# Kernel tuning notes

Hardware: AMD Instinct MI355X
Metric: run time of the kernel (lower is better)

## Reference

```python
import jax, jax.numpy as jnp
import numpy as np

DIM = 192
WH, WW = 8, 8
N = WH * WW
NUM_HEADS = 6
HEAD_DIM = DIM // NUM_HEADS
SCALE = HEAD_DIM ** (-0.5)
B_ = 4096


def _relative_position_index(Wh, Ww):
    coords = np.stack(np.meshgrid(np.arange(Wh), np.arange(Ww), indexing='ij'))  # [2, Wh, Ww]
    cf = coords.reshape(2, -1)                              # [2, N]
    rel = cf[:, :, None] - cf[:, None, :]                   # [2, N, N]
    rel = rel.transpose(1, 2, 0).astype(np.int64)           # [N, N, 2]
    rel[..., 0] += Wh - 1
    rel[..., 1] += Ww - 1
    rel[..., 0] *= 2 * Ww - 1
    return rel.sum(-1)                                      # [N, N]


REL_IDX = jnp.asarray(_relative_position_index(WH, WW))


def setup_inputs() -> dict:
    key = jax.random.key(0)
    ks = jax.random.split(key, 6)
    x = jax.random.normal(ks[0], (B_, N, DIM), dtype=jnp.float32)
    w_qkv = jax.random.normal(ks[1], (3 * DIM, DIM), dtype=jnp.float32) * (DIM ** -0.5)
    b_qkv = jnp.zeros((3 * DIM,), dtype=jnp.float32)
    w_proj = jax.random.normal(ks[2], (DIM, DIM), dtype=jnp.float32) * (DIM ** -0.5)
    b_proj = jnp.zeros((DIM,), dtype=jnp.float32)
    # torch init is zeros; use small noise so the bias path is exercised
    bias_table = jax.random.normal(ks[3], ((2 * WH - 1) * (2 * WW - 1), NUM_HEADS), dtype=jnp.float32) * 0.02
    return {"x": x, "w_qkv": w_qkv, "b_qkv": b_qkv, "w_proj": w_proj,
            "b_proj": b_proj, "bias_table": bias_table}


def reference(x, w_qkv, b_qkv, w_proj, b_proj, bias_table):
    B, n, C = x.shape
    qkv = jnp.einsum('bnc,dc->bnd', x, w_qkv) + b_qkv        # [B, N, 3C]
    qkv = qkv.reshape(B, n, 3, NUM_HEADS, HEAD_DIM)
    q = qkv[:, :, 0].transpose(0, 2, 1, 3) * SCALE            # [B, H, N, hd]
    k = qkv[:, :, 1].transpose(0, 2, 1, 3)
    v = qkv[:, :, 2].transpose(0, 2, 1, 3)
    attn = jnp.einsum('bhnd,bhmd->bhnm', q, k)                # [B, H, N, N]
    bias = bias_table[REL_IDX]                                # [N, N, H]
    attn = attn + bias.transpose(2, 0, 1)[None]               # broadcast over B
    attn = jax.nn.softmax(attn, axis=-1)
    out = jnp.einsum('bhnm,bhmd->bnhd', attn, v).reshape(B, n, C)
    return jnp.einsum('bnc,dc->bnd', out, w_proj) + b_proj
```

## Files before the change

kernel.cpp:

```cpp
#include <hip/hip_runtime.h>

#define TOK 64
#define CDIM 192
#define NH 6
#define HD 32
#define THREADS 768
#define QSCALE 0.17677669529663687f

#define WQ16_OFF 0
#define WP16_OFF 110592
#define BIAS_OFF 147456
#define WS_HALFS (147456 + 24576)
#define WS_BYTES (WS_HALFS * 2)

typedef _Float16 f16x8 __attribute__((ext_vector_type(8)));
typedef _Float16 f16x4 __attribute__((ext_vector_type(4)));
typedef float f32x4 __attribute__((ext_vector_type(4)));

__device__ __forceinline__ f16x8 ld8(const _Float16* p) {
  return *reinterpret_cast<const f16x8*>(p);
}

__device__ __forceinline__ f16x8 cvt8(const float* __restrict__ p) {
  float4 a = *reinterpret_cast<const float4*>(p);
  float4 c = *reinterpret_cast<const float4*>(p + 4);
  f16x8 r;
  r[0] = (_Float16)a.x; r[1] = (_Float16)a.y; r[2] = (_Float16)a.z; r[3] = (_Float16)a.w;
  r[4] = (_Float16)c.x; r[5] = (_Float16)c.y; r[6] = (_Float16)c.z; r[7] = (_Float16)c.w;
  return r;
}

__global__ void prep_ws(const float* __restrict__ wq, const float* __restrict__ wp,
                        const float* __restrict__ bt, _Float16* __restrict__ ws) {
  int i = blockIdx.x * 256 + threadIdx.x;
  if (i < 27648) {
    float4 v = reinterpret_cast<const float4*>(wq)[i];
    f16x4 h;
    h[0] = (_Float16)v.x; h[1] = (_Float16)v.y; h[2] = (_Float16)v.z; h[3] = (_Float16)v.w;
    *reinterpret_cast<f16x4*>(ws + WQ16_OFF + (size_t)i * 4) = h;
  } else if (i < 36864) {
    int j = i - 27648;
    float4 v = reinterpret_cast<const float4*>(wp)[j];
    f16x4 h;
    h[0] = (_Float16)v.x; h[1] = (_Float16)v.y; h[2] = (_Float16)v.z; h[3] = (_Float16)v.w;
    *reinterpret_cast<f16x4*>(ws + WP16_OFF + (size_t)j * 4) = h;
  } else if (i < 61440) {
    int j = i - 36864;
    int hit = j >> 10;
    int l = (j >> 4) & 63;
    int s = j & 15;
    int h = hit >> 2, it = hit & 3;
    int ii = it * 16 + (l & 15);
    int jj = (s >> 2) * 16 + (l >> 4) * 4 + (s & 3);
    int rel = ((ii >> 3) - (jj >> 3) + 7) * 15 + ((ii & 7) - (jj & 7) + 7);
    ws[BIAS_OFF + j] = (_Float16)bt[rel * NH + h];
  }
}

template <bool WS>
__global__ __launch_bounds__(THREADS, 6) void winattn(
    const float* __restrict__ x, const float* __restrict__ w_qkv,
    const float* __restrict__ b_qkv, const float* __restrict__ w_proj,
    const float* __restrict__ b_proj, const float* __restrict__ bias_table,
    const _Float16* __restrict__ ws, float* __restrict__ out) {
  __shared__ __align__(16) _Float16 R1[12288];
  __shared__ __align__(16) _Float16 R2[12288];

  const int tid = threadIdx.x;
  const int w   = tid >> 6;
  const int l   = tid & 63;
  const int l15 = l & 15;
  const int lg  = l >> 4;
  const int b   = blockIdx.x;
  const int h   = w >> 1;
  const int wh  = w & 1;
  const f32x4 vzero = {0.f, 0.f, 0.f, 0.f};

  const float* xg = x + (size_t)b * (TOK * CDIM);
#pragma unroll
  for (int i = tid; i < TOK * CDIM / 4; i += THREADS) {
    int n = i / (CDIM / 4);
    int c = (i % (CDIM / 4)) * 4;
    float4 v = reinterpret_cast<const float4*>(xg)[i];
    f16x4 h4;
    h4[0] = (_Float16)v.x; h4[1] = (_Float16)v.y;
    h4[2] = (_Float16)v.z; h4[3] = (_Float16)v.w;
    *reinterpret_cast<f16x4*>(&R1[((c >> 3) * TOK + n) * 8 + (c & 7)]) = h4;
  }
  __syncthreads();

  const int sdl = h * HD + wh * 16 + l15;
  const int hd  = wh * 16 + l15;

  f32x4 aq[4], ak[4];
#pragma unroll
  for (int mt = 0; mt < 4; ++mt) { aq[mt] = vzero; ak[mt] = vzero; }
#pragma unroll
  for (int ks = 0; ks < 6; ++ks) {
    f16x8 a[4];
#pragma unroll
    for (int mt = 0; mt < 4; ++mt)
      a[mt] = ld8(&R1[((ks * 4 + lg) * TOK + mt * 16 + l15) * 8]);
    f16x8 bfq, bfk;
    if constexpr (WS) {
      bfq = ld8(ws + WQ16_OFF + (size_t)sdl * CDIM + ks * 32 + lg * 8);
      bfk = ld8(ws + WQ16_OFF + (size_t)(CDIM + sdl) * CDIM + ks * 32 + lg * 8);
    } else {
      bfq = cvt8(w_qkv + (size_t)sdl * CDIM + ks * 32 + lg * 8);
      bfk = cvt8(w_qkv + (size_t)(CDIM + sdl) * CDIM + ks * 32 + lg * 8);
    }
#pragma unroll
    for (int mt = 0; mt < 4; ++mt) {
      aq[mt] = __builtin_amdgcn_mfma_f32_16x16x32_f16(a[mt], bfq, aq[mt], 0, 0, 0);
      ak[mt] = __builtin_amdgcn_mfma_f32_16x16x32_f16(a[mt], bfk, ak[mt], 0, 0, 0);
    }
  }
  {
    float bq1 = b_qkv[CDIM + sdl];
#pragma unroll
    for (int mt = 0; mt < 4; ++mt)
#pragma unroll
      for (int r = 0; r < 4; ++r) {
        int n = mt * 16 + lg * 4 + r;
        R2[h * 2048 + ((hd >> 3) * TOK + n) * 8 + (hd & 7)] = (_Float16)(ak[mt][r] + bq1);
      }
  }

  f32x4 av[4];
#pragma unroll
  for (int mt = 0; mt < 4; ++mt) av[mt] = vzero;
#pragma unroll
  for (int ks = 0; ks < 6; ++ks) {
    f16x8 a[4];
#pragma unroll
    for (int mt = 0; mt < 4; ++mt)
      a[mt] = ld8(&R1[((ks * 4 + lg) * TOK + mt * 16 + l15) * 8]);
    f16x8 bfv;
    if constexpr (WS) bfv = ld8(ws + WQ16_OFF + (size_t)(2 * CDIM + sdl) * CDIM + ks * 32 + lg * 8);
    else              bfv = cvt8(w_qkv + (size_t)(2 * CDIM + sdl) * CDIM + ks * 32 + lg * 8);
#pragma unroll
    for (int mt = 0; mt < 4; ++mt)
      av[mt] = __builtin_amdgcn_mfma_f32_16x16x32_f16(a[mt], bfv, av[mt], 0, 0, 0);
  }
  __syncthreads();

  f16x8 kf[4];
#pragma unroll
  for (int jt = 0; jt < 4; ++jt)
    kf[jt] = ld8(&R2[h * 2048 + (lg * TOK + jt * 16 + l15) * 8]);
  {
    float bq2 = b_qkv[2 * CDIM + sdl];
#pragma unroll
    for (int mt = 0; mt < 4; ++mt)
#pragma unroll
      for (int r = 0; r < 4; ++r) {
        int n = mt * 16 + lg * 4 + r;
        R1[h * 2048 + ((n >> 3) * HD + hd) * 8 + (n & 7)] = (_Float16)(av[mt][r] + bq2);
      }
  }
  __syncthreads();

  f16x8 vf[4];
#pragma unroll
  for (int z = 0; z < 4; ++z) {
    int ks = z >> 1, nt = z & 1;
    vf[z] = ld8(&R1[h * 2048 + ((ks * 4 + lg) * HD + nt * 16 + l15) * 8]);
  }
  {
    float bq0 = b_qkv[sdl];
#pragma unroll
    for (int mt = 0; mt < 4; ++mt)
#pragma unroll
      for (int r = 0; r < 4; ++r) {
        int n = mt * 16 + lg * 4 + r;
        R2[h * 2048 + ((hd >> 3) * TOK + n) * 8 + (hd & 7)] =
            (_Float16)((aq[mt][r] + bq0) * QSCALE);
      }
  }
  __syncthreads();

  f16x8 qf[2];
#pragma unroll
  for (int ii = 0; ii < 2; ++ii) {
    int it = wh * 2 + ii;
    qf[ii] = ld8(&R2[h * 2048 + (lg * TOK + it * 16 + l15) * 8]);
  }
  __syncthreads();

  {
    _Float16* pbase = &R2[w * 1024];
#pragma unroll
    for (int ii = 0; ii < 2; ++ii) {
      const int it = wh * 2 + ii;
      f32x4 st[4];
#pragma unroll
      for (int jt = 0; jt < 4; ++jt)
        st[jt] = __builtin_amdgcn_mfma_f32_16x16x32_f16(kf[jt], qf[ii], vzero, 0, 0, 0);
      if constexpr (WS) {
        const _Float16* bw = ws + BIAS_OFF + ((h * 4 + it) * 64 + l) * 16;
        f16x8 b0 = ld8(bw), b1 = ld8(bw + 8);
#pragma unroll
        for (int jt = 0; jt < 4; ++jt)
#pragma unroll
          for (int r = 0; r < 4; ++r)
            st[jt][r] += (float)((jt < 2) ? b0[jt * 4 + r] : b1[(jt - 2) * 4 + r]);
      } else {
        int i = it * 16 + l15, yi = i >> 3, xi = i & 7;
#pragma unroll
        for (int jt = 0; jt < 4; ++jt)
#pragma unroll
          for (int r = 0; r < 4; ++r) {
            int j = jt * 16 + lg * 4 + r, yj = j >> 3, xj = j & 7;
            st[jt][r] += bias_table[(((yi - yj + 7) * 15 + (xi - xj + 7)) * NH + h)];
          }
      }
      float m = st[0][0];
#pragma unroll
      for (int jt = 0; jt < 4; ++jt)
#pragma unroll
        for (int r = 0; r < 4; ++r) m = fmaxf(m, st[jt][r]);
      m = fmaxf(m, __shfl_xor(m, 16, 64));
      m = fmaxf(m, __shfl_xor(m, 32, 64));
      float sum = 0.f;
#pragma unroll
      for (int jt = 0; jt < 4; ++jt)
#pragma unroll
        for (int r = 0; r < 4; ++r) { st[jt][r] = __expf(st[jt][r] - m); sum += st[jt][r]; }
      sum += __shfl_xor(sum, 16, 64);
      sum += __shfl_xor(sum, 32, 64);
      float inv = 1.f / sum;
#pragma unroll
      for (int jt = 0; jt < 4; ++jt) {
        f16x4 pk;
#pragma unroll
        for (int r = 0; r < 4; ++r) pk[r] = (_Float16)(st[jt][r] * inv);
        *reinterpret_cast<f16x4*>(
            &pbase[((jt * 2 + (lg >> 1)) * 16 + l15) * 8 + (lg & 1) * 4]) = pk;
      }
      f32x4 o[2] = {vzero, vzero};
#pragma unroll
      for (int ks = 0; ks < 2; ++ks) {
        f16x8 pf = ld8(&pbase[((ks * 4 + lg) * 16 + l15) * 8]);
#pragma unroll
        for (int nt = 0; nt < 2; ++nt)
          o[nt] = __builtin_amdgcn_mfma_f32_16x16x32_f16(pf, vf[ks * 2 + nt], o[nt], 0, 0, 0);
      }
#pragma unroll
      for (int nt = 0; nt < 2; ++nt) {
        int c = h * HD + nt * 16 + l15;
#pragma unroll
        for (int r = 0; r < 4; ++r) {
          int i2 = it * 16 + lg * 4 + r;
          R1[((c >> 3) * TOK + i2) * 8 + (c & 7)] = (_Float16)o[nt][r];
        }
      }
    }
  }
  __syncthreads();

  {
    const int e = w * 16 + l15;
    f32x4 pacc[4];
#pragma unroll
    for (int mt = 0; mt < 4; ++mt) pacc[mt] = vzero;
#pragma unroll
    for (int ks = 0; ks < 6; ++ks) {
      f16x8 bf;
      if constexpr (WS) bf = ld8(ws + WP16_OFF + (size_t)e * CDIM + ks * 32 + lg * 8);
      else              bf = cvt8(w_proj + (size_t)e * CDIM + ks * 32 + lg * 8);
#pragma unroll
      for (int mt = 0; mt < 4; ++mt) {
        f16x8 a = ld8(&R1[((ks * 4 + lg) * TOK + mt * 16 + l15) * 8]);
        pacc[mt] = __builtin_amdgcn_mfma_f32_16x16x32_f16(a, bf, pacc[mt], 0, 0, 0);
      }
    }
    float bp = b_proj[e];
#pragma unroll
    for (int mt = 0; mt < 4; ++mt)
#pragma unroll
      for (int r = 0; r < 4; ++r) {
        int n = mt * 16 + lg * 4 + r;
        out[((size_t)b * TOK + n) * CDIM + e] = pacc[mt][r] + bp;
      }
  }
}

extern "C" void kernel_launch(void* const* d_in, const int* in_sizes, int n_in,
                              void* d_out, int out_size, void* d_ws, size_t ws_size,
                              hipStream_t stream) {
  const float* x          = (const float*)d_in[0];
  const float* w_qkv      = (const float*)d_in[1];
  const float* b_qkv      = (const float*)d_in[2];
  const float* w_proj     = (const float*)d_in[3];
  const float* b_proj     = (const float*)d_in[4];
  const float* bias_table = (const float*)d_in[5];
  float* out = (float*)d_out;
  int B = in_sizes[0] / (TOK * CDIM);

  if (ws_size >= (size_t)WS_BYTES) {
    _Float16* ws = (_Float16*)d_ws;
    hipLaunchKernelGGL(prep_ws, dim3(240), dim3(256), 0, stream,
                       w_qkv, w_proj, bias_table, ws);
    hipLaunchKernelGGL(winattn<true>, dim3(B), dim3(THREADS), 0, stream,
                       x, w_qkv, b_qkv, w_proj, b_proj, bias_table, ws, out);
  } else {
    hipLaunchKernelGGL(winattn<false>, dim3(B), dim3(THREADS), 0, stream,
                       x, w_qkv, b_qkv, w_proj, b_proj, bias_table,
                       (const _Float16*)nullptr, out);
  }
}
```

Baseline: 213.6 us.

## Swizzle LDS tile layouts to cut bank conflicts, add MFMA priority hints

Applies an XOR swizzle on the row index to every shared-memory tile (x, K, Q, V, attention output) and changes the matching reads and writes. The x staging loop now writes 8 halves per store, and the V store is vectorised to 4-half writes, so LDS bank conflicts and store count both drop. It also wraps the MFMA groups in s_setprio to favour matrix issue across waves. This adds index arithmetic, and any mismatch in the swizzle between writers and readers would corrupt results.

```diff
diff --git a/kernel.cpp b/kernel.cpp
--- a/kernel.cpp
+++ b/kernel.cpp
@@ -78,29 +78,36 @@
 
   const float* xg = x + (size_t)b * (TOK * CDIM);
 #pragma unroll
-  for (int i = tid; i < TOK * CDIM / 4; i += THREADS) {
-    int n = i / (CDIM / 4);
-    int c = (i % (CDIM / 4)) * 4;
-    float4 v = reinterpret_cast<const float4*>(xg)[i];
-    f16x4 h4;
-    h4[0] = (_Float16)v.x; h4[1] = (_Float16)v.y;
-    h4[2] = (_Float16)v.z; h4[3] = (_Float16)v.w;
-    *reinterpret_cast<f16x4*>(&R1[((c >> 3) * TOK + n) * 8 + (c & 7)]) = h4;
+  for (int kk = 0; kk < 2; ++kk) {
+    int q = tid + kk * 768;
+    int n = q / 24;
+    int p = q - n * 24;
+    const float* src = xg + q * 8;
+    float4 v0 = *reinterpret_cast<const float4*>(src);
+    float4 v1 = *reinterpret_cast<const float4*>(src + 4);
+    f16x8 h8;
+    h8[0] = (_Float16)v0.x; h8[1] = (_Float16)v0.y;
+    h8[2] = (_Float16)v0.z; h8[3] = (_Float16)v0.w;
+    h8[4] = (_Float16)v1.x; h8[5] = (_Float16)v1.y;
+    h8[6] = (_Float16)v1.z; h8[7] = (_Float16)v1.w;
+    *reinterpret_cast<f16x8*>(&R1[(p * TOK + (n ^ (p & 7))) * 8]) = h8;
   }
   __syncthreads();
 
   const int sdl = h * HD + wh * 16 + l15;
   const int hd  = wh * 16 + l15;
+  const int dp  = hd >> 3;
 
   f32x4 aq[4], ak[4];
 #pragma unroll
   for (int mt = 0; mt < 4; ++mt) { aq[mt] = vzero; ak[mt] = vzero; }
 #pragma unroll
   for (int ks = 0; ks < 6; ++ks) {
+    const int sp = (ks * 4) & 7;
     f16x8 a[4];
 #pragma unroll
     for (int mt = 0; mt < 4; ++mt)
-      a[mt] = ld8(&R1[((ks * 4 + lg) * TOK + mt * 16 + l15) * 8]);
+      a[mt] = ld8(&R1[((ks * 4 + lg) * TOK + ((mt * 16 + l15) ^ (sp + lg))) * 8]);
     f16x8 bfq, bfk;
     if constexpr (WS) {
       bfq = ld8(ws + WQ16_OFF + (size_t)sdl * CDIM + ks * 32 + lg * 8);
@@ -109,11 +116,13 @@
       bfq = cvt8(w_qkv + (size_t)sdl * CDIM + ks * 32 + lg * 8);
       bfk = cvt8(w_qkv + (size_t)(CDIM + sdl) * CDIM + ks * 32 + lg * 8);
     }
+    __builtin_amdgcn_s_setprio(1);
 #pragma unroll
     for (int mt = 0; mt < 4; ++mt) {
       aq[mt] = __builtin_amdgcn_mfma_f32_16x16x32_f16(a[mt], bfq, aq[mt], 0, 0, 0);
       ak[mt] = __builtin_amdgcn_mfma_f32_16x16x32_f16(a[mt], bfk, ak[mt], 0, 0, 0);
     }
+    __builtin_amdgcn_s_setprio(0);
   }
   {
     float bq1 = b_qkv[CDIM + sdl];
@@ -122,7 +131,7 @@
 #pragma unroll
       for (int r = 0; r < 4; ++r) {
         int n = mt * 16 + lg * 4 + r;
-        R2[h * 2048 + ((hd >> 3) * TOK + n) * 8 + (hd & 7)] = (_Float16)(ak[mt][r] + bq1);
+        R2[h * 2048 + (dp * TOK + (n ^ dp)) * 8 + (hd & 7)] = (_Float16)(ak[mt][r] + bq1);
       }
   }
 
@@ -131,49 +140,55 @@
   for (int mt = 0; mt < 4; ++mt) av[mt] = vzero;
 #pragma unroll
   for (int ks = 0; ks < 6; ++ks) {
+    const int sp = (ks * 4) & 7;
     f16x8 a[4];
 #pragma unroll
     for (int mt = 0; mt < 4; ++mt)
-      a[mt] = ld8(&R1[((ks * 4 + lg) * TOK + mt * 16 + l15) * 8]);
+      a[mt] = ld8(&R1[((ks * 4 + lg) * TOK + ((mt * 16 + l15) ^ (sp + lg))) * 8]);
     f16x8 bfv;
     if constexpr (WS) bfv = ld8(ws + WQ16_OFF + (size_t)(2 * CDIM + sdl) * CDIM + ks * 32 + lg * 8);
     else              bfv = cvt8(w_qkv + (size_t)(2 * CDIM + sdl) * CDIM + ks * 32 + lg * 8);
+    __builtin_amdgcn_s_setprio(1);
 #pragma unroll
     for (int mt = 0; mt < 4; ++mt)
       av[mt] = __builtin_amdgcn_mfma_f32_16x16x32_f16(a[mt], bfv, av[mt], 0, 0, 0);
+    __builtin_amdgcn_s_setprio(0);
   }
   __syncthreads();
 
   f16x8 kf[4];
 #pragma unroll
   for (int jt = 0; jt < 4; ++jt)
-    kf[jt] = ld8(&R2[h * 2048 + (lg * TOK + jt * 16 + l15) * 8]);
+    kf[jt] = ld8(&R2[h * 2048 + (lg * TOK + ((jt * 16 + l15) ^ lg)) * 8]);
   {
     float bq2 = b_qkv[2 * CDIM + sdl];
+#pragma unroll
+    for (int mt = 0; mt < 4; ++mt) {
+      int vp = 2 * mt + (lg >> 1);
+      f16x4 pk;
+#pragma unroll
+      for (int r = 0; r < 4; ++r) pk[r] = (_Float16)(av[mt][r] + bq2);
+      *reinterpret_cast<f16x4*>(
+          &R1[h * 2048 + (vp * HD + (hd ^ vp)) * 8 + (lg & 1) * 4]) = pk;
+    }
+  }
+  __syncthreads();
+
+  f16x8 vf[4];
+#pragma unroll
+  for (int z = 0; z < 4; ++z) {
+    int ks = z >> 1, nt = z & 1;
+    int tp = ks * 4 + lg;
+    vf[z] = ld8(&R1[h * 2048 + (tp * HD + ((nt * 16 + l15) ^ tp)) * 8]);
+  }
+  {
+    float bq0 = b_qkv[sdl];
 #pragma unroll
     for (int mt = 0; mt < 4; ++mt)
 #pragma unroll
       for (int r = 0; r < 4; ++r) {
         int n = mt * 16 + lg * 4 + r;
-        R1[h * 2048 + ((n >> 3) * HD + hd) * 8 + (n & 7)] = (_Float16)(av[mt][r] + bq2);
-      }
-  }
-  __syncthreads();
-
-  f16x8 vf[4];
-#pragma unroll
-  for (int z = 0; z < 4; ++z) {
-    int ks = z >> 1, nt = z & 1;
-    vf[z] = ld8(&R1[h * 2048 + ((ks * 4 + lg) * HD + nt * 16 + l15) * 8]);
-  }
-  {
-    float bq0 = b_qkv[sdl];
-#pragma unroll
-    for (int mt = 0; mt < 4; ++mt)
-#pragma unroll
-      for (int r = 0; r < 4; ++r) {
-        int n = mt * 16 + lg * 4 + r;
-        R2[h * 2048 + ((hd >> 3) * TOK + n) * 8 + (hd & 7)] =
+        R2[h * 2048 + (dp * TOK + (n ^ dp)) * 8 + (hd & 7)] =
             (_Float16)((aq[mt][r] + bq0) * QSCALE);
       }
   }
@@ -183,7 +198,7 @@
 #pragma unroll
   for (int ii = 0; ii < 2; ++ii) {
     int it = wh * 2 + ii;
-    qf[ii] = ld8(&R2[h * 2048 + (lg * TOK + it * 16 + l15) * 8]);
+    qf[ii] = ld8(&R2[h * 2048 + (lg * TOK + ((it * 16 + l15) ^ lg)) * 8]);
   }
   __syncthreads();
 
@@ -193,9 +208,11 @@
     for (int ii = 0; ii < 2; ++ii) {
       const int it = wh * 2 + ii;
       f32x4 st[4];
+      __builtin_amdgcn_s_setprio(1);
 #pragma unroll
       for (int jt = 0; jt < 4; ++jt)
         st[jt] = __builtin_amdgcn_mfma_f32_16x16x32_f16(kf[jt], qf[ii], vzero, 0, 0, 0);
+      __builtin_amdgcn_s_setprio(0);
       if constexpr (WS) {
         const _Float16* bw = ws + BIAS_OFF + ((h * 4 + it) * 64 + l) * 16;
         f16x8 b0 = ld8(bw), b1 = ld8(bw + 8);
@@ -241,17 +258,20 @@
 #pragma unroll
       for (int ks = 0; ks < 2; ++ks) {
         f16x8 pf = ld8(&pbase[((ks * 4 + lg) * 16 + l15) * 8]);
+        __builtin_amdgcn_s_setprio(1);
 #pragma unroll
         for (int nt = 0; nt < 2; ++nt)
           o[nt] = __builtin_amdgcn_mfma_f32_16x16x32_f16(pf, vf[ks * 2 + nt], o[nt], 0, 0, 0);
+        __builtin_amdgcn_s_setprio(0);
       }
 #pragma unroll
       for (int nt = 0; nt < 2; ++nt) {
         int c = h * HD + nt * 16 + l15;
+        int op = c >> 3;
 #pragma unroll
         for (int r = 0; r < 4; ++r) {
           int i2 = it * 16 + lg * 4 + r;
-          R1[((c >> 3) * TOK + i2) * 8 + (c & 7)] = (_Float16)o[nt][r];
+          R1[(op * TOK + (i2 ^ (op & 7))) * 8 + (c & 7)] = (_Float16)o[nt][r];
         }
       }
     }
@@ -265,14 +285,19 @@
     for (int mt = 0; mt < 4; ++mt) pacc[mt] = vzero;
 #pragma unroll
     for (int ks = 0; ks < 6; ++ks) {
+      const int sp = (ks * 4) & 7;
       f16x8 bf;
       if constexpr (WS) bf = ld8(ws + WP16_OFF + (size_t)e * CDIM + ks * 32 + lg * 8);
       else              bf = cvt8(w_proj + (size_t)e * CDIM + ks * 32 + lg * 8);
-#pragma unroll
-      for (int mt = 0; mt < 4; ++mt) {
-        f16x8 a = ld8(&R1[((ks * 4 + lg) * TOK + mt * 16 + l15) * 8]);
-        pacc[mt] = __builtin_amdgcn_mfma_f32_16x16x32_f16(a, bf, pacc[mt], 0, 0, 0);
-      }
+      f16x8 a[4];
+#pragma unroll
+      for (int mt = 0; mt < 4; ++mt)
+        a[mt] = ld8(&R1[((ks * 4 + lg) * TOK + ((mt * 16 + l15) ^ (sp + lg))) * 8]);
+      __builtin_amdgcn_s_setprio(1);
+#pragma unroll
+      for (int mt = 0; mt < 4; ++mt)
+        pacc[mt] = __builtin_amdgcn_mfma_f32_16x16x32_f16(a[mt], bf, pacc[mt], 0, 0, 0);
+      __builtin_amdgcn_s_setprio(0);
     }
     float bp = b_proj[e];
 #pragma unroll
```

After: 394.6 us. 84.7% more time.
